# Kernel tuning notes

Hardware: AMD Instinct MI355X
Metric: run time of the kernel (lower is better)

## Reference

```python
import jax, jax.numpy as jnp
import numpy as np

B, CIN, COUT, T, H, W, NH = 8, 16, 16, 32, 16, 16, 4
DIN = CIN * H * W    # 4096
DOUT = COUT * H * W  # 4096
DH = DOUT // NH      # 1024


def conv3d(x, w, b, pad):
    y = jax.lax.conv_general_dilated(
        x, w, window_strides=(1, 1, 1), padding=((pad, pad),) * 3,
        dimension_numbers=('NCDHW', 'OIDHW', 'NCDHW'))
    return y + b[None, :, None, None, None]


def instance_norm(x, eps=1e-5):
    # InstanceNorm3d default: no affine, normalize per (B,C) over (T,H,W)
    mu = x.mean(axis=(2, 3, 4), keepdims=True)
    var = ((x - mu) ** 2).mean(axis=(2, 3, 4), keepdims=True)
    return (x - mu) * jax.lax.rsqrt(var + eps)


def slstm(x, Wg, bg, Rg):
    # x: (B,T,D). Wg: (4,D,D) input weights [i,f,z,o]; bg: (4,D);
    # Rg: (NH,4,DH,DH) block-diagonal per-head recurrent weights.
    Bb, Tt, D = x.shape
    Gx = jnp.einsum('btd,god->btgo', x, Wg) + bg  # (B,T,4,D)

    def step(carry, gx):
        h, c, n, m = carry
        hh = h.reshape(Bb, NH, DH)
        gh = jnp.einsum('bhd,hgod->bhgo', hh, Rg)          # (B,NH,4,DH)
        pre = gx + gh.transpose(0, 2, 1, 3).reshape(Bb, 4, D)
        i_pre, f_pre, z_pre, o_pre = pre[:, 0], pre[:, 1], pre[:, 2], pre[:, 3]
        # stabilized exponential gating (xLSTM sLSTM)
        m_new = jnp.maximum(f_pre + m, i_pre)
        i = jnp.exp(i_pre - m_new)
        f = jnp.exp(f_pre + m - m_new)
        c = f * c + i * jnp.tanh(z_pre)
        n = f * n + i
        h = jax.nn.sigmoid(o_pre) * c / n
        return (h, c, n, m_new), h

    init = tuple(jnp.zeros((Bb, D), x.dtype) for _ in range(4))
    _, hs = jax.lax.scan(step, init, Gx.transpose(1, 0, 2, 3))  # hs: (T,B,D)
    return hs.transpose(1, 0, 2)


def setup_inputs():
    key = jax.random.key(0)
    ks = jax.random.split(key, 8)
    s = 0.02
    return {
        'x': jax.random.normal(ks[0], (B, CIN, T, H, W), jnp.float32),
        'c1_w': jax.random.normal(ks[1], (COUT, CIN, 3, 3, 3), jnp.float32) * 0.05,
        'c1_b': jnp.zeros((COUT,), jnp.float32),
        'c2_w': jax.random.normal(ks[2], (COUT, COUT, 3, 3, 3), jnp.float32) * 0.05,
        'c2_b': jnp.zeros((COUT,), jnp.float32),
        'c3_w': jax.random.normal(ks[3], (COUT, COUT, 3, 3, 3), jnp.float32) * 0.05,
        'c3_b': jnp.zeros((COUT,), jnp.float32),
        'pre_w': jax.random.normal(ks[4], (DOUT, DIN), jnp.float32) * s,
        'pre_b': jnp.zeros((DOUT,), jnp.float32),
        'lstm_W': jax.random.normal(ks[5], (4, DOUT, DOUT), jnp.float32) * s,
        'lstm_b': jnp.zeros((4, DOUT), jnp.float32),
        'lstm_R': jax.random.normal(ks[6], (NH, 4, DH, DH), jnp.float32) * s,
        'attn_w': jax.random.normal(ks[7], (1, 2 * COUT), jnp.float32) * 0.05,
        'attn_b': jnp.zeros((1,), jnp.float32),
    }


def reference(x, c1_w, c1_b, c2_w, c2_b, c3_w, c3_b, pre_w, pre_b,
              lstm_W, lstm_b, lstm_R, attn_w, attn_b):
    # conv3d branch: conv -> IN -> relu -> conv -> relu -> conv -> relu
    y = jax.nn.relu(instance_norm(conv3d(x, c1_w, c1_b, 1)))
    y = jax.nn.relu(conv3d(y, c2_w, c2_b, 1))
    out3d = jax.nn.relu(conv3d(y, c3_w, c3_b, 1))
    # sLSTM branch
    xs = x.transpose(0, 2, 1, 3, 4).reshape(B, T, DIN)
    xs = xs @ pre_w.T + pre_b
    hs = slstm(xs, lstm_W, lstm_b, lstm_R)                 # (B,T,DOUT)
    s_out = hs.reshape(B, T, COUT, H, W).transpose(0, 2, 1, 3, 4)
    # attention-gated fusion: cat -> 1x1x1 conv -> sigmoid -> weighted sum
    comb = jnp.concatenate([s_out, out3d], axis=1)         # (B,2*COUT,T,H,W)
    alpha = jax.nn.sigmoid(jnp.einsum('bcthw,oc->bothw', comb, attn_w)
                           + attn_b[None, :, None, None, None])
    return alpha * out3d + (1 - alpha) * s_out
```

## Files before the change

kernel.cpp:

```cpp
#include <hip/hip_runtime.h>
#include <hip/hip_bf16.h>
#include <cstddef>

#define BB   8
#define CIN  16
#define COUT 16
#define TT   32
#define HH   16
#define WW   16
#define DIN  4096
#define DOUT 4096
#define NH   4
#define DH   1024
#define SPAT 8192
#define NSEQ 256

typedef __attribute__((ext_vector_type(8))) short  bf16x8;
typedef __attribute__((ext_vector_type(4))) float  f32x4;
typedef __attribute__((ext_vector_type(4))) unsigned short us4;
typedef __attribute__((ext_vector_type(4))) int    i32x4;
typedef unsigned short ushort_t;
typedef unsigned long long u64_t;

static __device__ __forceinline__ ushort_t f2bf(float f) {
    union { float f; unsigned u; } v; v.f = f;
    unsigned r = (v.u + 0x7fffu + ((v.u >> 16) & 1u)) >> 16;
    return (ushort_t)r;
}
static __device__ __forceinline__ float bf2f(ushort_t u) {
    union { unsigned u; float f; } v; v.u = ((unsigned)u) << 16;
    return v.f;
}

__global__ void setup_kernel(const float* __restrict__ x, ushort_t* __restrict__ xt,
                             const float* __restrict__ w1, const float* __restrict__ w2,
                             const float* __restrict__ w3,
                             float* __restrict__ cw1, float* __restrict__ cw2,
                             float* __restrict__ cw3, int* __restrict__ flags) {
    int bid = blockIdx.x;
    if (bid < 1024) {
        int idx = bid * 256 + threadIdx.x;
        int n = idx >> 10, k4 = (idx & 1023) * 4;
        int b = n >> 5, t = n & 31, c = k4 >> 8, hw = k4 & 255;
        f32x4 f = *(const f32x4*)&x[(((size_t)(b * CIN + c) * TT + t)) * 256 + hw];
        us4 o;
        #pragma unroll
        for (int i = 0; i < 4; ++i) o[i] = f2bf(f[i]);
        *(us4*)&xt[(size_t)n * DIN + k4] = o;
    } else if (bid < 1105) {
        int i = (bid - 1024) * 256 + threadIdx.x;
        if (i < 3 * 6912) {
            int set = i / 6912, j = i - set * 6912;
            const float* w = (set == 0) ? w1 : (set == 1) ? w2 : w3;
            float* cw      = (set == 0) ? cw1 : (set == 1) ? cw2 : cw3;
            int o = j & 15, r = j >> 4;
            int k = r % 27, ci = r / 27;
            cw[j] = w[(size_t)(o * CIN + ci) * 27 + k];
        }
    } else {
        int j = (bid - 1105) * 256 + threadIdx.x;
        if (j < 2176)
            ((i32x4*)flags)[j] = (i32x4){0, 0, 0, 0};
    }
}

template<int BN, int BK, bool OUT_BF16>
__device__ __forceinline__
void gemm_body(char* smem, int bx,
               const ushort_t* __restrict__ A, const float* __restrict__ B,
               const float* __restrict__ bias, void* __restrict__ C,
               int N, int K) {
    constexpr int NF  = BN / 16;
    constexpr int TPR = 256 / BN;
    constexpr int FPT = BK / TPR;
    ushort_t* Al = (ushort_t*)smem;
    ushort_t* Bl = Al + 2 * 256 * BK;
    int tid  = threadIdx.x;
    int lane = tid & 63;
    int wv   = tid >> 6;
    int n0 = bx * BN;

    f32x4 acc[4][NF];
    #pragma unroll
    for (int i = 0; i < 4; ++i)
        #pragma unroll
        for (int j = 0; j < NF; ++j) acc[i][j] = (f32x4){0.f, 0.f, 0.f, 0.f};

    auto stageA = [&](int buf, int k0) {
        #pragma unroll
        for (int q = 0; q < 8; ++q) {
            int rbase = wv * 64 + q * 8;
            int row = rbase + (lane >> 3);
            const ushort_t* g = A + (size_t)row * K + k0 + (lane & 7) * 8;
            __builtin_amdgcn_global_load_lds(
                (const __attribute__((address_space(1))) void*)g,
                (__attribute__((address_space(3))) void*)&Al[(buf * 256 + rbase) * BK],
                16, 0, 0);
        }
    };
    auto stageB = [&](int buf, int k0) {
        int r  = tid / TPR;
        int cs = (tid % TPR) * FPT;
        const float* g = B + (size_t)(n0 + r) * K + k0 + cs;
        #pragma unroll
        for (int q = 0; q < FPT / 4; ++q) {
            f32x4 f = *(const f32x4*)(g + q * 4);
            us4 pk;
            #pragma unroll
            for (int e = 0; e < 4; ++e) pk[e] = f2bf(f[e]);
            *(us4*)&Bl[(buf * BN + r) * BK + cs + q * 4] = pk;
        }
    };
    auto compute = [&](int buf) {
        #pragma unroll
        for (int ks = 0; ks < BK / 32; ++ks) {
            bf16x8 af[4], bfr[NF];
            #pragma unroll
            for (int i = 0; i < 4; ++i)
                af[i] = *(const bf16x8*)&Al[(buf * 256 + wv * 64 + i * 16 + (lane & 15)) * BK + ks * 32 + (lane >> 4) * 8];
            #pragma unroll
            for (int j = 0; j < NF; ++j)
                bfr[j] = *(const bf16x8*)&Bl[(buf * BN + j * 16 + (lane & 15)) * BK + ks * 32 + (lane >> 4) * 8];
            #pragma unroll
            for (int i = 0; i < 4; ++i)
                #pragma unroll
                for (int j = 0; j < NF; ++j)
                    acc[i][j] = __builtin_amdgcn_mfma_f32_16x16x32_bf16(af[i], bfr[j], acc[i][j], 0, 0, 0);
        }
    };

    stageA(0, 0); stageB(0, 0);
    __syncthreads();
    int nk = K / BK;
    int cur = 0;
    for (int t = 0; t < nk; ++t) {
        if (t + 1 < nk) { stageA(cur ^ 1, (t + 1) * BK); stageB(cur ^ 1, (t + 1) * BK); }
        compute(cur);
        __syncthreads();
        cur ^= 1;
    }

    #pragma unroll
    for (int i = 0; i < 4; ++i) {
        int row = wv * 64 + i * 16 + (lane >> 4) * 4;
        #pragma unroll
        for (int j = 0; j < NF; ++j) {
            int col = n0 + j * 16 + (lane & 15);
            float bv = bias[col];
            #pragma unroll
            for (int r = 0; r < 4; ++r) {
                float v = acc[i][j][r] + bv;
                if constexpr (OUT_BF16) ((ushort_t*)C)[(size_t)(row + r) * N + col] = f2bf(v);
                else                    ((float*)C)[(size_t)(row + r) * N + col] = v;
            }
        }
    }
}

__device__ __forceinline__
void conv_taps(const float* xin, const float* __restrict__ cw, int half,
               const float* __restrict__ bias, float* accs, int tid) {
    int h = tid >> 4, wx = tid & 15;
    f32x4 a0 = *(const f32x4*)&bias[half * 8];
    f32x4 a1 = *(const f32x4*)&bias[half * 8 + 4];
    for (int ci = 0; ci < CIN; ++ci) {
        #pragma unroll
        for (int kt = 0; kt < 3; ++kt) {
            #pragma unroll
            for (int kh = 0; kh < 3; ++kh) {
                int h2 = h + kh - 1;
                bool vh = (unsigned)h2 < HH;
                int h2c = vh ? h2 : 0;
                #pragma unroll
                for (int kw = 0; kw < 3; ++kw) {
                    int w2 = wx + kw - 1;
                    bool v = vh && ((unsigned)w2 < WW);
                    int w2c = ((unsigned)w2 < WW) ? w2 : 0;
                    float xv = xin[(ci * 3 + kt) * 256 + h2c * 16 + w2c];
                    xv = v ? xv : 0.f;
                    const float* wp = cw + (size_t)(ci * 27 + kt * 9 + kh * 3 + kw) * 16 + half * 8;
                    f32x4 w0 = *(const f32x4*)(wp);
                    f32x4 w1 = *(const f32x4*)(wp + 4);
                    a0 += xv * w0; a1 += xv * w1;
                }
            }
        }
    }
    #pragma unroll
    for (int i = 0; i < 4; ++i) { accs[i] = a0[i]; accs[4 + i] = a1[i]; }
}

__device__ __forceinline__
void conv1_body(char* smem, int blk,
                const float* __restrict__ in, const float* __restrict__ cw,
                const float* __restrict__ bias,
                float* __restrict__ out, float* __restrict__ psum) {
    float* xin = (float*)smem;
    int b = blk >> 6, t = (blk >> 1) & 31, half = blk & 1;
    int tid = threadIdx.x;

    for (int i = tid; i < CIN * 3 * 256; i += 256) {
        int hw = i & 255, r = i >> 8;
        int kt = r % 3, ci = r / 3;
        int tt = t + kt - 1;
        float v = 0.f;
        if ((unsigned)tt < TT)
            v = in[((size_t)(b * CIN + ci) * TT + tt) * 256 + hw];
        xin[(ci * 3 + kt) * 256 + hw] = v;
    }
    __syncthreads();

    float accs[8];
    conv_taps(xin, cw, half, bias, accs, tid);
    #pragma unroll
    for (int o = 0; o < 8; ++o)
        out[((size_t)(b * COUT + half * 8 + o) * TT + t) * 256 + tid] = accs[o];

    __syncthreads();
    float* sm = xin;
    int wv = tid >> 6;
    #pragma unroll
    for (int o = 0; o < 8; ++o) {
        float s = accs[o];
        float q = accs[o] * accs[o];
        #pragma unroll
        for (int m = 1; m < 64; m <<= 1) {
            s += __shfl_xor(s, m, 64);
            q += __shfl_xor(q, m, 64);
        }
        if ((tid & 63) == 0) { sm[wv * 16 + o * 2] = s; sm[wv * 16 + o * 2 + 1] = q; }
    }
    __syncthreads();
    if (tid < 16) {
        int o = tid >> 1, which = tid & 1;
        float v = sm[o * 2 + which] + sm[16 + o * 2 + which]
                + sm[32 + o * 2 + which] + sm[48 + o * 2 + which];
        psum[((((size_t)(b * 32 + t) * 2 + half) * 8 + o) * 2) + which] = v;
    }
}

__device__ __forceinline__
void conv2_body(char* smem, int blk,
                const float* __restrict__ y1, const float* __restrict__ cw,
                const float* __restrict__ bias, const float* __restrict__ psum,
                float* __restrict__ y2, int* __restrict__ cflags) {
    float* xin = (float*)smem;
    float* sstats = xin + 12288;
    int b = blk >> 6, t = (blk >> 1) & 31, half = blk & 1;
    int tid = threadIdx.x;

    if (tid < 16) {
        int c = tid;
        float sum = 0.f, sq = 0.f;
        for (int t2 = 0; t2 < 32; ++t2) {
            size_t base = (((size_t)(b * 32 + t2) * 2 + (c >> 3)) * 8 + (c & 7)) * 2;
            sum += psum[base];
            sq  += psum[base + 1];
        }
        float mu = sum / (float)SPAT;
        float var = sq / (float)SPAT - mu * mu;
        sstats[c * 2]     = mu;
        sstats[c * 2 + 1] = rsqrtf(var + 1e-5f);
    }
    __syncthreads();

    for (int i = tid; i < CIN * 3 * 256; i += 256) {
        int hw = i & 255, r = i >> 8;
        int kt = r % 3, ci = r / 3;
        int tt = t + kt - 1;
        float v = 0.f;
        if ((unsigned)tt < TT) {
            v = y1[((size_t)(b * CIN + ci) * TT + tt) * 256 + hw];
            v = fmaxf((v - sstats[ci * 2]) * sstats[ci * 2 + 1], 0.f);
        }
        xin[(ci * 3 + kt) * 256 + hw] = v;
    }
    __syncthreads();

    float accs[8];
    conv_taps(xin, cw, half, bias, accs, tid);
    #pragma unroll
    for (int o = 0; o < 8; ++o) {
        float v = fmaxf(accs[o], 0.f);
        __hip_atomic_store(&y2[((size_t)(b * COUT + half * 8 + o) * TT + t) * 256 + tid],
                           v, __ATOMIC_RELAXED, __HIP_MEMORY_SCOPE_AGENT);
    }
    __syncthreads();
    if (tid == 0)
        __hip_atomic_store(&cflags[blk], 1, __ATOMIC_RELAXED, __HIP_MEMORY_SCOPE_AGENT);
}

__device__ __forceinline__
void conv3_body(char* smem, int blk,
                const float* __restrict__ y2, const float* __restrict__ cw,
                const float* __restrict__ bias, float* __restrict__ out3d,
                const int* __restrict__ cflags) {
    float* xin = (float*)smem;
    int b = blk >> 6, t = (blk >> 1) & 31, half = blk & 1;
    int tid = threadIdx.x;

    if (tid == 0) {
        #pragma unroll
        for (int dt = -1; dt <= 1; ++dt) {
            int tn = t + dt;
            if ((unsigned)tn >= TT) continue;
            #pragma unroll
            for (int hh = 0; hh < 2; ++hh) {
                const int* f = &cflags[(b << 6) | (tn << 1) | hh];
                while (__hip_atomic_load(f, __ATOMIC_RELAXED,
                                         __HIP_MEMORY_SCOPE_AGENT) == 0)
                    __builtin_amdgcn_s_sleep(1);
            }
        }
    }
    __syncthreads();

    for (int i = tid; i < CIN * 3 * 256; i += 256) {
        int hw = i & 255, r = i >> 8;
        int kt = r % 3, ci = r / 3;
        int tt = t + kt - 1;
        float v = 0.f;
        if ((unsigned)tt < TT)
            v = __hip_atomic_load(&y2[((size_t)(b * CIN + ci) * TT + tt) * 256 + hw],
                                  __ATOMIC_RELAXED, __HIP_MEMORY_SCOPE_AGENT);
        xin[(ci * 3 + kt) * 256 + hw] = v;
    }
    __syncthreads();

    float accs[8];
    conv_taps(xin, cw, half, bias, accs, tid);
    #pragma unroll
    for (int o = 0; o < 8; ++o)
        out3d[((size_t)(b * COUT + half * 8 + o) * TT + t) * 256 + tid] = fmaxf(accs[o], 0.f);
}

__global__ __launch_bounds__(256, 2)
void fused1_kernel(const ushort_t* __restrict__ xt, const float* __restrict__ pre_w,
                   const float* __restrict__ pre_b, ushort_t* __restrict__ xs2b,
                   const float* __restrict__ x, const float* __restrict__ cw1,
                   const float* __restrict__ c1_b, float* __restrict__ y1,
                   float* __restrict__ psum) {
    extern __shared__ char smem[];
    if (blockIdx.x < 64)
        gemm_body<64, 64, true>(smem, blockIdx.x, xt, pre_w, pre_b, xs2b, DOUT, DIN);
    else
        conv1_body(smem, blockIdx.x - 64, x, cw1, c1_b, y1, psum);
}

__global__ __launch_bounds__(256, 2)
void fused2_kernel(const ushort_t* __restrict__ xs2b, const float* __restrict__ lstm_W,
                   const float* __restrict__ lstm_b, float* __restrict__ Gx,
                   const float* __restrict__ y1, const float* __restrict__ cw2,
                   const float* __restrict__ c2_b, const float* __restrict__ psum,
                   float* __restrict__ y2,
                   const float* __restrict__ cw3, const float* __restrict__ c3_b,
                   float* __restrict__ out3d, int* __restrict__ cflags) {
    extern __shared__ char smem[];
    if (blockIdx.x < 256)
        gemm_body<64, 64, false>(smem, blockIdx.x, xs2b, lstm_W, lstm_b, Gx, 4 * DOUT, DOUT);
    else if (blockIdx.x < 768)
        conv2_body(smem, blockIdx.x - 256, y1, cw2, c2_b, psum, y2, cflags);
    else
        conv3_body(smem, blockIdx.x - 768, y2, cw3, c3_b, out3d, cflags);
}

__global__ __launch_bounds__(256, 1)
void lstm_persist_kernel(const float* __restrict__ R,
                         const float* __restrict__ Gx,
                         unsigned* __restrict__ hfr,
                         int* __restrict__ flags,
                         const float* __restrict__ out3d,
                         const float* __restrict__ attn_w,
                         const float* __restrict__ attn_b,
                         float* __restrict__ out) {
    __shared__ ushort_t Rl[4][32][64 * 8];
    __shared__ float gh_p[4][4][16][8];

    int tid  = threadIdx.x;
    int lane = tid & 63;
    int w    = tid >> 6;
    int head = blockIdx.x >> 6;
    int oc   = blockIdx.x & 63;

    #pragma unroll 4
    for (int n = 0; n < 64; ++n) {
        int g = n >> 4, r = n & 15;
        const float* src = R + ((size_t)((head * 4 + g) * DH + oc * 16 + r)) * DH + tid * 4;
        f32x4 f = *(const f32x4*)src;
        int k0 = tid * 4;
        int ks = k0 >> 5;
        int kI = (k0 >> 3) & 3;
        int e8 = k0 & 7;
        union { ushort_t u[4]; u64_t q; } pk;
        #pragma unroll
        for (int e = 0; e < 4; ++e) pk.u[e] = f2bf(f[e]);
        *(u64_t*)&Rl[g][ks][((kI << 4) | r) * 8 + e8] = pk.q;
    }

    int arow = lane & 15;
    int part = arow >> 3;
    int bb   = arow & 7;
    int kseg = lane >> 4;

    int gb  = tid >> 4;
    int gol = tid & 15;
    int gd  = head * DH + oc * 16 + gol;
    int o_h = oc * 16 + gol;
    unsigned hslot = ((unsigned)head * 32 + (o_h >> 5)) * 256 + gb * 32 + (o_h & 31);
    float c_r = 0.f, n_r = 0.f, m_r = 0.f;

    __syncthreads();

    for (int t = 0; t < TT; ++t) {
        float gx0 = 0.f, gx1 = 0.f, gx2 = 0.f, gx3 = 0.f;
        if (tid < 128) {
            size_t gxoff = ((size_t)(gb * TT + t)) * (4 * DOUT) + gd;
            gx0 = Gx[gxoff];
            gx1 = Gx[gxoff + DOUT];
            gx2 = Gx[gxoff + 2 * DOUT];
            gx3 = Gx[gxoff + 3 * DOUT];
        }

        if (t > 0) {
            const int* fl = flags + (((t - 1) * 4 + head) << 6);
            for (;;) {
                int v = __hip_atomic_load(fl + lane, __ATOMIC_RELAXED,
                                          __HIP_MEMORY_SCOPE_AGENT);
                if (__all(v != 0)) break;
                __builtin_amdgcn_s_sleep(1);
            }

            const u64_t* hb = (const u64_t*)hfr
                + ((((size_t)(t - 1) * 4 + head) * 32) * 256 + bb * 32 + kseg * 8) / 2;
            bf16x8 hf[8];
            #pragma unroll
            for (int j = 0; j < 8; ++j) {
                const u64_t* p = hb + (size_t)(w * 8 + j) * 128;
                union { ushort_t u[8]; bf16x8 v; } fr;
                #pragma unroll
                for (int e2 = 0; e2 < 4; ++e2) {
                    u64_t q = __hip_atomic_load(p + e2, __ATOMIC_RELAXED,
                                                __HIP_MEMORY_SCOPE_AGENT);
                    unsigned q0 = (unsigned)q, q1 = (unsigned)(q >> 32);
                    fr.u[e2 * 2]     = part ? (ushort_t)(q0 >> 16) : (ushort_t)(q0 & 0xffffu);
                    fr.u[e2 * 2 + 1] = part ? (ushort_t)(q1 >> 16) : (ushort_t)(q1 & 0xffffu);
                }
                hf[j] = fr.v;
            }

            f32x4 acc[4];
            #pragma unroll
            for (int g = 0; g < 4; ++g) acc[g] = (f32x4){0.f, 0.f, 0.f, 0.f};
            #pragma unroll
            for (int g = 0; g < 4; ++g)
                #pragma unroll
                for (int j = 0; j < 8; ++j) {
                    bf16x8 a = *(const bf16x8*)&Rl[g][w * 8 + j][lane * 8];
                    acc[g] = __builtin_amdgcn_mfma_f32_16x16x32_bf16(a, hf[j], acc[g], 0, 0, 0);
                }
            #pragma unroll
            for (int g = 0; g < 4; ++g)
                #pragma unroll
                for (int r = 0; r < 4; ++r)
                    acc[g][r] += __shfl_xor(acc[g][r], 8, 64);
            if (part == 0) {
                int orow0 = kseg * 4;
                #pragma unroll
                for (int g = 0; g < 4; ++g)
                    #pragma unroll
                    for (int r = 0; r < 4; ++r)
                        gh_p[w][g][orow0 + r][bb] = acc[g][r];
            }
        } else {
            for (int i = tid; i < 4 * 4 * 16 * 8; i += 256)
                ((float*)gh_p)[i] = 0.f;
        }
        __syncthreads();

        if (tid < 128) {
            float ip = gx0 +
                gh_p[0][0][gol][gb] + gh_p[1][0][gol][gb] + gh_p[2][0][gol][gb] + gh_p[3][0][gol][gb];
            float fp = gx1 +
                gh_p[0][1][gol][gb] + gh_p[1][1][gol][gb] + gh_p[2][1][gol][gb] + gh_p[3][1][gol][gb];
            float zp = gx2 +
                gh_p[0][2][gol][gb] + gh_p[1][2][gol][gb] + gh_p[2][2][gol][gb] + gh_p[3][2][gol][gb];
            float op = gx3 +
                gh_p[0][3][gol][gb] + gh_p[1][3][gol][gb] + gh_p[2][3][gol][gb] + gh_p[3][3][gol][gb];
            float mn = fmaxf(fp + m_r, ip);
            float iv = __expf(ip - mn);
            float fv = __expf(fp + m_r - mn);
            float zc = fminf(fmaxf(zp, -9.f), 9.f);
            float th = 1.f - 2.f / (__expf(2.f * zc) + 1.f);
            c_r = fv * c_r + iv * th;
            n_r = fv * n_r + iv;
            float sig = 1.f / (1.f + __expf(-op));
            float hv = sig * c_r / n_r;
            m_r = mn;
            unsigned hi = f2bf(hv);
            unsigned lo = f2bf(hv - bf2f((ushort_t)hi));
            __hip_atomic_store(&hfr[(size_t)t * 32768 + hslot],
                               hi | (lo << 16),
                               __ATOMIC_RELAXED, __HIP_MEMORY_SCOPE_AGENT);
        }
        __syncthreads();
        if (tid == 0)
            __hip_atomic_store(&flags[((t * 4 + head) << 6) + oc], 1,
                               __ATOMIC_RELAXED, __HIP_MEMORY_SCOPE_AGENT);
    }

    {
        const int* fl31 = flags + ((31 * 4) << 6);
        for (;;) {
            int ok = 1;
            #pragma unroll
            for (int q = 0; q < 4; ++q)
                ok &= (__hip_atomic_load(fl31 + q * 64 + lane, __ATOMIC_RELAXED,
                                         __HIP_MEMORY_SCOPE_AGENT) != 0);
            if (__all(ok)) break;
            __builtin_amdgcn_s_sleep(1);
        }

        int idx = blockIdx.x * 256 + tid;
        int hw = idx & 255;
        int tC = (idx >> 8) & 31;
        int bC = idx >> 13;
        float dot = attn_b[0];
        float sv[16], ov[16];
        #pragma unroll
        for (int ch = 0; ch < 16; ++ch) {
            int d = ch * 256 + hw;
            int hd2 = d >> 10, o_h2 = d & 1023;
            size_t slot = (size_t)tC * 32768 + (size_t)hd2 * 8192
                        + (o_h2 >> 5) * 256 + bC * 32 + (o_h2 & 31);
            unsigned v32 = __hip_atomic_load(&hfr[slot], __ATOMIC_RELAXED,
                                             __HIP_MEMORY_SCOPE_AGENT);
            float s = bf2f((ushort_t)(v32 & 0xffffu)) + bf2f((ushort_t)(v32 >> 16));
            float o3 = out3d[(((size_t)(bC * COUT + ch) * TT + tC)) * 256 + hw];
            sv[ch] = s; ov[ch] = o3;
            dot += attn_w[ch] * s + attn_w[16 + ch] * o3;
        }
        float alpha = 1.f / (1.f + expf(-dot));
        #pragma unroll
        for (int ch = 0; ch < 16; ++ch) {
            out[(((size_t)(bC * COUT + ch) * TT + tC)) * 256 + hw] =
                alpha * ov[ch] + (1.f - alpha) * sv[ch];
        }
    }
}

extern "C" void kernel_launch(void* const* d_in, const int* in_sizes, int n_in,
                              void* d_out, int out_size, void* d_ws, size_t ws_size,
                              hipStream_t stream) {
    const float* x      = (const float*)d_in[0];
    const float* c1_w   = (const float*)d_in[1];
    const float* c1_b   = (const float*)d_in[2];
    const float* c2_w   = (const float*)d_in[3];
    const float* c2_b   = (const float*)d_in[4];
    const float* c3_w   = (const float*)d_in[5];
    const float* c3_b   = (const float*)d_in[6];
    const float* pre_w  = (const float*)d_in[7];
    const float* pre_b  = (const float*)d_in[8];
    const float* lstm_W = (const float*)d_in[9];
    const float* lstm_b = (const float*)d_in[10];
    const float* lstm_R = (const float*)d_in[11];
    const float* attn_w = (const float*)d_in[12];
    const float* attn_b = (const float*)d_in[13];
    float* out = (float*)d_out;

    float* wsf = (float*)d_ws;
    float* y1    = wsf;
    float* y2    = y1 + 1048576;
    float* out3d = y2 + 1048576;
    float* Gx    = out3d + 1048576;
    float* cw1   = Gx + 4194304;
    float* cw2   = cw1 + 6912;
    float* cw3   = cw2 + 6912;
    float* psum  = cw3 + 6912;
    float* pad   = psum + 8192;
    ushort_t* xt   = (ushort_t*)(pad + 64);
    ushort_t* xs2b = xt + 1048576;
    unsigned* hfr  = (unsigned*)(xs2b + 1048576);
    int*     flags = (int*)(hfr + 1048576);
    int*    cflags = flags + 8192;

    setup_kernel<<<1114, 256, 0, stream>>>(x, xt, c1_w, c2_w, c3_w, cw1, cw2, cw3, flags);

    fused1_kernel<<<576, 256, 81920, stream>>>(xt, pre_w, pre_b, xs2b,
                                               x, cw1, c1_b, y1, psum);

    fused2_kernel<<<1280, 256, 81920, stream>>>(xs2b, lstm_W, lstm_b, Gx,
                                                y1, cw2, c2_b, psum, y2,
                                                cw3, c3_b, out3d, cflags);

    lstm_persist_kernel<<<256, 256, 0, stream>>>(lstm_R, Gx, hfr, flags,
                                                 out3d, attn_w, attn_b, out);
}
```

Baseline: 526.6 us.

## Merge Gx GEMM, conv2/3 and persistent sLSTM into one flag-synchronized mega kernel

Folds the second fused kernel (input-gate GEMM plus conv2 and conv3) and the persistent sLSTM kernel into a single launch. Per-block readiness flags (gxflags) and a conv3 completion counter replace the kernel boundary. Persistent LSTM blocks can load their recurrent weights and begin as soon as their Gx tiles are ready, instead of waiting for all conv work to finish. In exchange, the kernel requests 139 KB of dynamic LDS with launch bounds of 1, which halves residency for the GEMM and conv blocks. It also adds spin-waiting, atomic loads and stores, and relies on in-order block dispatch so the later persistent blocks do not block producers.

```diff
diff --git a/kernel.cpp b/kernel.cpp
--- a/kernel.cpp
+++ b/kernel.cpp
@@ -59,12 +59,12 @@
         }
     } else {
         int j = (bid - 1105) * 256 + threadIdx.x;
-        if (j < 2176)
+        if (j < 2241)
             ((i32x4*)flags)[j] = (i32x4){0, 0, 0, 0};
     }
 }
 
-template<int BN, int BK, bool OUT_BF16>
+template<int BN, int BK, bool OUT_BF16, bool ATOMIC_OUT>
 __device__ __forceinline__
 void gemm_body(char* smem, int bx,
                const ushort_t* __restrict__ A, const float* __restrict__ B,
@@ -150,8 +150,13 @@
             #pragma unroll
             for (int r = 0; r < 4; ++r) {
                 float v = acc[i][j][r] + bv;
-                if constexpr (OUT_BF16) ((ushort_t*)C)[(size_t)(row + r) * N + col] = f2bf(v);
-                else                    ((float*)C)[(size_t)(row + r) * N + col] = v;
+                if constexpr (OUT_BF16)
+                    ((ushort_t*)C)[(size_t)(row + r) * N + col] = f2bf(v);
+                else if constexpr (ATOMIC_OUT)
+                    __hip_atomic_store(&((float*)C)[(size_t)(row + r) * N + col], v,
+                                       __ATOMIC_RELAXED, __HIP_MEMORY_SCOPE_AGENT);
+                else
+                    ((float*)C)[(size_t)(row + r) * N + col] = v;
             }
         }
     }
@@ -331,56 +336,27 @@
     conv_taps(xin, cw, half, bias, accs, tid);
     #pragma unroll
     for (int o = 0; o < 8; ++o)
-        out3d[((size_t)(b * COUT + half * 8 + o) * TT + t) * 256 + tid] = fmaxf(accs[o], 0.f);
-}
-
-__global__ __launch_bounds__(256, 2)
-void fused1_kernel(const ushort_t* __restrict__ xt, const float* __restrict__ pre_w,
-                   const float* __restrict__ pre_b, ushort_t* __restrict__ xs2b,
-                   const float* __restrict__ x, const float* __restrict__ cw1,
-                   const float* __restrict__ c1_b, float* __restrict__ y1,
-                   float* __restrict__ psum) {
-    extern __shared__ char smem[];
-    if (blockIdx.x < 64)
-        gemm_body<64, 64, true>(smem, blockIdx.x, xt, pre_w, pre_b, xs2b, DOUT, DIN);
-    else
-        conv1_body(smem, blockIdx.x - 64, x, cw1, c1_b, y1, psum);
-}
-
-__global__ __launch_bounds__(256, 2)
-void fused2_kernel(const ushort_t* __restrict__ xs2b, const float* __restrict__ lstm_W,
-                   const float* __restrict__ lstm_b, float* __restrict__ Gx,
-                   const float* __restrict__ y1, const float* __restrict__ cw2,
-                   const float* __restrict__ c2_b, const float* __restrict__ psum,
-                   float* __restrict__ y2,
-                   const float* __restrict__ cw3, const float* __restrict__ c3_b,
-                   float* __restrict__ out3d, int* __restrict__ cflags) {
-    extern __shared__ char smem[];
-    if (blockIdx.x < 256)
-        gemm_body<64, 64, false>(smem, blockIdx.x, xs2b, lstm_W, lstm_b, Gx, 4 * DOUT, DOUT);
-    else if (blockIdx.x < 768)
-        conv2_body(smem, blockIdx.x - 256, y1, cw2, c2_b, psum, y2, cflags);
-    else
-        conv3_body(smem, blockIdx.x - 768, y2, cw3, c3_b, out3d, cflags);
-}
-
-__global__ __launch_bounds__(256, 1)
-void lstm_persist_kernel(const float* __restrict__ R,
-                         const float* __restrict__ Gx,
-                         unsigned* __restrict__ hfr,
-                         int* __restrict__ flags,
-                         const float* __restrict__ out3d,
-                         const float* __restrict__ attn_w,
-                         const float* __restrict__ attn_b,
-                         float* __restrict__ out) {
-    __shared__ ushort_t Rl[4][32][64 * 8];
-    __shared__ float gh_p[4][4][16][8];
+        __hip_atomic_store(&out3d[((size_t)(b * COUT + half * 8 + o) * TT + t) * 256 + tid],
+                           fmaxf(accs[o], 0.f),
+                           __ATOMIC_RELAXED, __HIP_MEMORY_SCOPE_AGENT);
+}
+
+__device__ __forceinline__
+void persist_body(char* smem, int pb,
+                  const float* __restrict__ R, const float* __restrict__ Gx,
+                  unsigned* __restrict__ hfr, int* __restrict__ flags,
+                  const int* __restrict__ gxflags, const int* __restrict__ c3done,
+                  const float* __restrict__ out3d,
+                  const float* __restrict__ attn_w, const float* __restrict__ attn_b,
+                  float* __restrict__ out) {
+    ushort_t* Rl = (ushort_t*)smem;
+    float* gh_p  = (float*)(smem + 131072);
 
     int tid  = threadIdx.x;
     int lane = tid & 63;
     int w    = tid >> 6;
-    int head = blockIdx.x >> 6;
-    int oc   = blockIdx.x & 63;
+    int head = pb >> 6;
+    int oc   = pb & 63;
 
     #pragma unroll 4
     for (int n = 0; n < 64; ++n) {
@@ -394,7 +370,18 @@
         union { ushort_t u[4]; u64_t q; } pk;
         #pragma unroll
         for (int e = 0; e < 4; ++e) pk.u[e] = f2bf(f[e]);
-        *(u64_t*)&Rl[g][ks][((kI << 4) | r) * 8 + e8] = pk.q;
+        *(u64_t*)&Rl[((g * 32 + ks) << 9) + ((kI << 4) | r) * 8 + e8] = pk.q;
+    }
+
+    {
+        for (;;) {
+            int v = 1;
+            if (lane < 4)
+                v = __hip_atomic_load(&gxflags[lane * 64 + head * 16 + (oc >> 2)],
+                                      __ATOMIC_RELAXED, __HIP_MEMORY_SCOPE_AGENT);
+            if (__all(v != 0)) break;
+            __builtin_amdgcn_s_sleep(1);
+        }
     }
 
     int arow = lane & 15;
@@ -415,10 +402,10 @@
         float gx0 = 0.f, gx1 = 0.f, gx2 = 0.f, gx3 = 0.f;
         if (tid < 128) {
             size_t gxoff = ((size_t)(gb * TT + t)) * (4 * DOUT) + gd;
-            gx0 = Gx[gxoff];
-            gx1 = Gx[gxoff + DOUT];
-            gx2 = Gx[gxoff + 2 * DOUT];
-            gx3 = Gx[gxoff + 3 * DOUT];
+            gx0 = __hip_atomic_load(&Gx[gxoff],            __ATOMIC_RELAXED, __HIP_MEMORY_SCOPE_AGENT);
+            gx1 = __hip_atomic_load(&Gx[gxoff + DOUT],     __ATOMIC_RELAXED, __HIP_MEMORY_SCOPE_AGENT);
+            gx2 = __hip_atomic_load(&Gx[gxoff + 2 * DOUT], __ATOMIC_RELAXED, __HIP_MEMORY_SCOPE_AGENT);
+            gx3 = __hip_atomic_load(&Gx[gxoff + 3 * DOUT], __ATOMIC_RELAXED, __HIP_MEMORY_SCOPE_AGENT);
         }
 
         if (t > 0) {
@@ -455,7 +442,7 @@
             for (int g = 0; g < 4; ++g)
                 #pragma unroll
                 for (int j = 0; j < 8; ++j) {
-                    bf16x8 a = *(const bf16x8*)&Rl[g][w * 8 + j][lane * 8];
+                    bf16x8 a = *(const bf16x8*)&Rl[((g * 32 + w * 8 + j) << 9) + lane * 8];
                     acc[g] = __builtin_amdgcn_mfma_f32_16x16x32_bf16(a, hf[j], acc[g], 0, 0, 0);
                 }
             #pragma unroll
@@ -469,23 +456,27 @@
                 for (int g = 0; g < 4; ++g)
                     #pragma unroll
                     for (int r = 0; r < 4; ++r)
-                        gh_p[w][g][orow0 + r][bb] = acc[g][r];
+                        gh_p[(((w * 4 + g) * 16 + orow0 + r) << 3) + bb] = acc[g][r];
             }
         } else {
             for (int i = tid; i < 4 * 4 * 16 * 8; i += 256)
-                ((float*)gh_p)[i] = 0.f;
+                gh_p[i] = 0.f;
         }
         __syncthreads();
 
         if (tid < 128) {
             float ip = gx0 +
-                gh_p[0][0][gol][gb] + gh_p[1][0][gol][gb] + gh_p[2][0][gol][gb] + gh_p[3][0][gol][gb];
+                gh_p[(((0 * 4 + 0) * 16 + gol) << 3) + gb] + gh_p[(((1 * 4 + 0) * 16 + gol) << 3) + gb] +
+                gh_p[(((2 * 4 + 0) * 16 + gol) << 3) + gb] + gh_p[(((3 * 4 + 0) * 16 + gol) << 3) + gb];
             float fp = gx1 +
-                gh_p[0][1][gol][gb] + gh_p[1][1][gol][gb] + gh_p[2][1][gol][gb] + gh_p[3][1][gol][gb];
+                gh_p[(((0 * 4 + 1) * 16 + gol) << 3) + gb] + gh_p[(((1 * 4 + 1) * 16 + gol) << 3) + gb] +
+                gh_p[(((2 * 4 + 1) * 16 + gol) << 3) + gb] + gh_p[(((3 * 4 + 1) * 16 + gol) << 3) + gb];
             float zp = gx2 +
-                gh_p[0][2][gol][gb] + gh_p[1][2][gol][gb] + gh_p[2][2][gol][gb] + gh_p[3][2][gol][gb];
+                gh_p[(((0 * 4 + 2) * 16 + gol) << 3) + gb] + gh_p[(((1 * 4 + 2) * 16 + gol) << 3) + gb] +
+                gh_p[(((2 * 4 + 2) * 16 + gol) << 3) + gb] + gh_p[(((3 * 4 + 2) * 16 + gol) << 3) + gb];
             float op = gx3 +
-                gh_p[0][3][gol][gb] + gh_p[1][3][gol][gb] + gh_p[2][3][gol][gb] + gh_p[3][3][gol][gb];
+                gh_p[(((0 * 4 + 3) * 16 + gol) << 3) + gb] + gh_p[(((1 * 4 + 3) * 16 + gol) << 3) + gb] +
+                gh_p[(((2 * 4 + 3) * 16 + gol) << 3) + gb] + gh_p[(((3 * 4 + 3) * 16 + gol) << 3) + gb];
             float mn = fmaxf(fp + m_r, ip);
             float iv = __expf(ip - mn);
             float fv = __expf(fp + m_r - mn);
@@ -519,8 +510,14 @@
             if (__all(ok)) break;
             __builtin_amdgcn_s_sleep(1);
         }
-
-        int idx = blockIdx.x * 256 + tid;
+        if (tid == 0) {
+            while (__hip_atomic_load(c3done, __ATOMIC_RELAXED,
+                                     __HIP_MEMORY_SCOPE_AGENT) < 512)
+                __builtin_amdgcn_s_sleep(1);
+        }
+        __syncthreads();
+
+        int idx = pb * 256 + tid;
         int hw = idx & 255;
         int tC = (idx >> 8) & 31;
         int bC = idx >> 13;
@@ -535,7 +532,8 @@
             unsigned v32 = __hip_atomic_load(&hfr[slot], __ATOMIC_RELAXED,
                                              __HIP_MEMORY_SCOPE_AGENT);
             float s = bf2f((ushort_t)(v32 & 0xffffu)) + bf2f((ushort_t)(v32 >> 16));
-            float o3 = out3d[(((size_t)(bC * COUT + ch) * TT + tC)) * 256 + hw];
+            float o3 = __hip_atomic_load(&out3d[(((size_t)(bC * COUT + ch) * TT + tC)) * 256 + hw],
+                                         __ATOMIC_RELAXED, __HIP_MEMORY_SCOPE_AGENT);
             sv[ch] = s; ov[ch] = o3;
             dot += attn_w[ch] * s + attn_w[16 + ch] * o3;
         }
@@ -545,6 +543,52 @@
             out[(((size_t)(bC * COUT + ch) * TT + tC)) * 256 + hw] =
                 alpha * ov[ch] + (1.f - alpha) * sv[ch];
         }
+    }
+}
+
+__global__ __launch_bounds__(256, 2)
+void fused1_kernel(const ushort_t* __restrict__ xt, const float* __restrict__ pre_w,
+                   const float* __restrict__ pre_b, ushort_t* __restrict__ xs2b,
+                   const float* __restrict__ x, const float* __restrict__ cw1,
+                   const float* __restrict__ c1_b, float* __restrict__ y1,
+                   float* __restrict__ psum) {
+    extern __shared__ char smem[];
+    if (blockIdx.x < 64)
+        gemm_body<64, 64, true, false>(smem, blockIdx.x, xt, pre_w, pre_b, xs2b, DOUT, DIN);
+    else
+        conv1_body(smem, blockIdx.x - 64, x, cw1, c1_b, y1, psum);
+}
+
+__global__ __launch_bounds__(256, 1)
+void mega_kernel(const ushort_t* __restrict__ xs2b, const float* __restrict__ lstm_W,
+                 const float* __restrict__ lstm_b, float* __restrict__ Gx,
+                 int* __restrict__ gxflags,
+                 const float* __restrict__ y1, const float* __restrict__ cw2,
+                 const float* __restrict__ c2_b, const float* __restrict__ psum,
+                 float* __restrict__ y2, int* __restrict__ cflags,
+                 const float* __restrict__ cw3, const float* __restrict__ c3_b,
+                 float* __restrict__ out3d, int* __restrict__ c3done,
+                 const float* __restrict__ R, unsigned* __restrict__ hfr,
+                 int* __restrict__ flags,
+                 const float* __restrict__ attn_w, const float* __restrict__ attn_b,
+                 float* __restrict__ out) {
+    extern __shared__ char smem[];
+    int bid = blockIdx.x;
+    if (bid < 256) {
+        gemm_body<64, 64, false, true>(smem, bid, xs2b, lstm_W, lstm_b, Gx, 4 * DOUT, DOUT);
+        __syncthreads();
+        if (threadIdx.x == 0)
+            __hip_atomic_store(&gxflags[bid], 1, __ATOMIC_RELAXED, __HIP_MEMORY_SCOPE_AGENT);
+    } else if (bid < 768) {
+        conv2_body(smem, bid - 256, y1, cw2, c2_b, psum, y2, cflags);
+    } else if (bid < 1280) {
+        conv3_body(smem, bid - 768, y2, cw3, c3_b, out3d, cflags);
+        __syncthreads();
+        if (threadIdx.x == 0)
+            __hip_atomic_fetch_add(c3done, 1, __ATOMIC_RELAXED, __HIP_MEMORY_SCOPE_AGENT);
+    } else {
+        persist_body(smem, bid - 1280, R, Gx, hfr, flags, gxflags, c3done,
+                     out3d, attn_w, attn_b, out);
     }
 }
 
@@ -582,16 +626,17 @@
     unsigned* hfr  = (unsigned*)(xs2b + 1048576);
     int*     flags = (int*)(hfr + 1048576);
     int*    cflags = flags + 8192;
+    int*   gxflags = cflags + 512;
+    int*    c3done = gxflags + 256;
 
     setup_kernel<<<1114, 256, 0, stream>>>(x, xt, c1_w, c2_w, c3_w, cw1, cw2, cw3, flags);
 
     fused1_kernel<<<576, 256, 81920, stream>>>(xt, pre_w, pre_b, xs2b,
                                                x, cw1, c1_b, y1, psum);
 
-    fused2_kernel<<<1280, 256, 81920, stream>>>(xs2b, lstm_W, lstm_b, Gx,
-                                                y1, cw2, c2_b, psum, y2,
-                                                cw3, c3_b, out3d, cflags);
-
-    lstm_persist_kernel<<<256, 256, 0, stream>>>(lstm_R, Gx, hfr, flags,
-                                                 out3d, attn_w, attn_b, out);
-}
+    mega_kernel<<<1536, 256, 139264, stream>>>(xs2b, lstm_W, lstm_b, Gx, gxflags,
+                                               y1, cw2, c2_b, psum, y2, cflags,
+                                               cw3, c3_b, out3d, c3done,
+                                               lstm_R, hfr, flags,
+                                               attn_w, attn_b, out);
+}
```

Result: slower. 651.6 us (+23.7%).
